# Kernel optimization log

Measured on AMD Instinct MI355X. Metric: run time of the kernel, lower is better.

Reference implementation:

```python
import jax, jax.numpy as jnp
import numpy as np

N_MEMBERS = 2      # ensemble_length=3, loop runs i=1..2
N_NODES = 65536    # batch_size * total_length = 32 * 2048
N_EDGES = 1_048_576
N_LAYERS = 12      # num_conv_layers
D = 64             # constant feature width (linspace 64->64)


def setup_inputs() -> dict:
    key = jax.random.key(0)
    k0, k1, k2, k3 = jax.random.split(key, 4)
    x = jax.random.normal(k0, (N_MEMBERS, N_NODES, D), dtype=jnp.float32)
    edge_index = jax.random.randint(k1, (N_MEMBERS, 2, N_EDGES), 0, N_NODES, dtype=jnp.int64)
    # GCNConv weights per member/layer; scale ~ 1/sqrt(D) for stability across 12 layers
    W = jax.random.normal(k2, (N_MEMBERS, N_LAYERS, D, D), dtype=jnp.float32) / jnp.sqrt(jnp.float32(D))
    b = jax.random.normal(k3, (N_MEMBERS, N_LAYERS, D), dtype=jnp.float32) * 0.01
    return {"x": x, "edge_index": edge_index, "W": W, "b": b}


def gcn_conv(h, src, dst, W, b):
    """PyG GCNConv: add self-loops, symmetric D^-1/2 (A+I) D^-1/2 normalization,
    linear transform, bias."""
    hw = h @ W                                                # [N, D_out]
    # degree includes the self-loop (+1)
    deg = jax.ops.segment_sum(jnp.ones((src.shape[0],), h.dtype), dst,
                              num_segments=N_NODES) + jnp.asarray(1.0, h.dtype)
    dinv = jax.lax.rsqrt(deg)                                 # [N]
    norm = dinv[src] * dinv[dst]                              # [E]
    agg = jax.ops.segment_sum(norm[:, None] * hw[src], dst, num_segments=N_NODES)
    agg = agg + (dinv * dinv)[:, None] * hw                   # self-loop term
    return agg + b


def reference(x, edge_index, W, b):
    # eval mode: F.dropout(training=False) is identity
    outs = []
    for i in range(N_MEMBERS):
        src, dst = edge_index[i, 0], edge_index[i, 1]
        h = x[i]
        for j in range(N_LAYERS - 1):
            h = jax.nn.relu(gcn_conv(h, src, dst, W[i, j], b[i, j]))
        outs.append(gcn_conv(h, src, dst, W[i, N_LAYERS - 1], b[i, N_LAYERS - 1]))
    return jnp.stack(outs)  # [N_MEMBERS, N_NODES, D]
```

## Files before the change

kernel.cpp:

```cpp
#include <hip/hip_runtime.h>
#include <hip/hip_fp16.h>
#include <math.h>

#define N_MEMBERS 2
#define N_NODES   65536
#define N_EDGES   1048576
#define N_LAYERS  12
#define D         64
#define OFF_STRIDE (N_NODES + 1)
#define NODE_MASK (N_NODES - 1)

#define NBINS       256
#define BIN_CAP     5120
#define EDGES_PER_WG 4096

typedef _Float16 f16;
typedef f16   f16x8 __attribute__((ext_vector_type(8)));
typedef float f32x4 __attribute__((ext_vector_type(4)));


__global__ __launch_bounds__(256) void bin_scatter_k(const int* __restrict__ ei,
                                                     int* __restrict__ binCursor,
                                                     unsigned int* __restrict__ binned) {
    int m = blockIdx.y;
    int t = threadIdx.x;
    int eBase = blockIdx.x * EDGES_PER_WG;
    __shared__ int hist[NBINS];
    __shared__ int base[NBINS];
    hist[t] = 0;
    __syncthreads();
    const int* srcp = ei + (size_t)(m * 2 + 0) * N_EDGES;
    const int* dstp = ei + (size_t)(m * 2 + 1) * N_EDGES;
    unsigned int pk[16];
    int bn[16], rk[16];
    #pragma unroll
    for (int i = 0; i < 16; i++) {
        int e = eBase + i * 256 + t;
        int src = srcp[e] & NODE_MASK;
        int dst = dstp[e] & NODE_MASK;
        int b = dst >> 8;
        bn[i] = b;
        pk[i] = ((unsigned)src << 8) | (unsigned)(dst & 255);
        rk[i] = atomicAdd(&hist[b], 1);
    }
    __syncthreads();
    base[t] = atomicAdd(&binCursor[m * NBINS + t], hist[t]);
    __syncthreads();
    unsigned int* bb = binned + (size_t)m * NBINS * BIN_CAP;
    #pragma unroll
    for (int i = 0; i < 16; i++) {
        int pos = base[bn[i]] + rk[i];
        if (pos < BIN_CAP)
            bb[(size_t)bn[i] * BIN_CAP + pos] = pk[i];
    }
}

__global__ __launch_bounds__(256) void scan_bins_k(const int* __restrict__ cur,
                                                   int* __restrict__ bbase) {
    int m = blockIdx.x, t = threadIdx.x;
    __shared__ int sh[256];
    int v0 = cur[m * NBINS + t];
    sh[t] = v0;
    __syncthreads();
    for (int ofs = 1; ofs < 256; ofs <<= 1) {
        int v = sh[t];
        int a = (t >= ofs) ? sh[t - ofs] : 0;
        __syncthreads();
        sh[t] = v + a;
        __syncthreads();
    }
    bbase[m * NBINS + t] = sh[t] - v0;
}

__global__ __launch_bounds__(256) void bin_build_k(const unsigned int* __restrict__ binned,
                                                   const int* __restrict__ binCursor,
                                                   const int* __restrict__ bbase,
                                                   int* __restrict__ off,
                                                   float* __restrict__ dinv,
                                                   unsigned short* __restrict__ csr_src) {
    int m = blockIdx.y, b = blockIdx.x, t = threadIdx.x;
    int cnt   = binCursor[m * NBINS + b];
    int gbase = bbase[m * NBINS + b];
    const unsigned int* bb = binned + ((size_t)m * NBINS + b) * BIN_CAP;
    __shared__ int degl[256];
    __shared__ int offl[256];
    degl[t] = 0;
    __syncthreads();
    unsigned int ed[20];
    #pragma unroll
    for (int j = 0; j < 20; j++) {
        int i = t + j * 256;
        ed[j] = 0;
        if (i < cnt) {
            unsigned int w = bb[i];
            int r = atomicAdd(&degl[w & 255], 1);
            ed[j] = w | ((unsigned)r << 24);
        }
    }
    __syncthreads();
    int myDeg = degl[t];
    offl[t] = myDeg;
    __syncthreads();
    for (int ofs = 1; ofs < 256; ofs <<= 1) {
        int v = offl[t];
        int a = (t >= ofs) ? offl[t - ofs] : 0;
        __syncthreads();
        offl[t] = v + a;
        __syncthreads();
    }
    int myOff = gbase + offl[t] - myDeg;
    int node = b * 256 + t;
    off[m * OFF_STRIDE + node] = myOff;
    if (b == NBINS - 1 && t == 255) off[m * OFF_STRIDE + N_NODES] = N_EDGES;
    dinv[m * N_NODES + node] = 1.0f / sqrtf((float)myDeg + 1.0f);
    offl[t] = myOff;
    __syncthreads();
    unsigned short* cs = csr_src + (size_t)m * N_EDGES;
    #pragma unroll
    for (int j = 0; j < 20; j++) {
        int i = t + j * 256;
        if (i < cnt) {
            int dl  = ed[j] & 255;
            int src = (ed[j] >> 8) & 0xFFFF;
            int r   = ed[j] >> 24;
            cs[offl[dl] + r] = (unsigned short)src;
        }
    }
}

__global__ __launch_bounds__(256) void prescale_k(const float* __restrict__ x,
                                                  const float* __restrict__ dinv,
                                                  __half* __restrict__ g) {
    int i = blockIdx.x * 256 + threadIdx.x;
    float dv = dinv[i >> 3];
    float4 a = ((const float4*)x)[i * 2];
    float4 b = ((const float4*)x)[i * 2 + 1];
    union { __half2 h2[4]; uint4 u; } p;
    p.h2[0] = __floats2half2_rn(dv * a.x, dv * a.y);
    p.h2[1] = __floats2half2_rn(dv * a.z, dv * a.w);
    p.h2[2] = __floats2half2_rn(dv * b.x, dv * b.y);
    p.h2[3] = __floats2half2_rn(dv * b.z, dv * b.w);
    ((uint4*)g)[i] = p.u;
}

__device__ __forceinline__ void cvt8(uint4 u, float* f) {
    const __half2* h2 = (const __half2*)&u;
    #pragma unroll
    for (int i = 0; i < 4; i++) {
        float2 t = __half22float2(h2[i]);
        f[2 * i]     = t.x;
        f[2 * i + 1] = t.y;
    }
}

__global__ __launch_bounds__(256) void aggregate_k(const __half* __restrict__ g,
                                                   __half* __restrict__ S,
                                                   const int* __restrict__ off,
                                                   const unsigned short* __restrict__ csr_src,
                                                   const float* __restrict__ dinv) {
    int m = blockIdx.y;
    int n = blockIdx.x * 4 + (threadIdx.x >> 6);
    int lane = threadIdx.x & 63;
    int fg   = lane & 7;
    int sub  = lane >> 3;
    const __half*         gm = g + (size_t)m * N_NODES * D;
    const int*            ob = off + m * OFF_STRIDE;
    const unsigned short* sb = csr_src + (size_t)m * N_EDGES;

    float acc[8];
    #pragma unroll
    for (int i = 0; i < 8; i++) acc[i] = 0.f;

    int e0 = ob[n], e1 = ob[n + 1];
    #pragma unroll 2
    for (int e = e0; e < e1; e += 8) {
        int ee  = e + sub;
        int idx = (ee < e1) ? ee : (e1 - 1);
        int s   = sb[idx];
        float w = (ee < e1) ? 1.0f : 0.0f;
        uint4 gv = *(const uint4*)(gm + (size_t)s * D + fg * 8);
        float f[8];
        cvt8(gv, f);
        #pragma unroll
        for (int i = 0; i < 8; i++) acc[i] = fmaf(w, f[i], acc[i]);
    }
    #pragma unroll
    for (int msk = 8; msk < 64; msk <<= 1)
        #pragma unroll
        for (int i = 0; i < 8; i++) acc[i] += __shfl_xor(acc[i], msk);

    float dv = dinv[m * N_NODES + n];
    uint4 sg = *(const uint4*)(gm + (size_t)n * D + fg * 8);
    float sf[8];
    cvt8(sg, sf);
    if (sub == 0) {
        union { __half2 h2[4]; uint4 u; } p;
        #pragma unroll
        for (int i = 0; i < 4; i++)
            p.h2[i] = __floats2half2_rn(dv * (acc[2 * i]     + sf[2 * i]),
                                        dv * (acc[2 * i + 1] + sf[2 * i + 1]));
        *(uint4*)(S + (size_t)m * N_NODES * D + (size_t)n * D + fg * 8) = p.u;
    }
}

__global__ __launch_bounds__(256) void gemm_f16_k(const __half* __restrict__ S,
                                                  const float* __restrict__ Wall,
                                                  const float* __restrict__ dinv,
                                                  const float* __restrict__ ball,
                                                  __half* __restrict__ gout,
                                                  float* __restrict__ fout,
                                                  int layer, int last) {
    int m = blockIdx.y;
    const float* Wg = Wall + (size_t)(m * N_LAYERS + layer) * D * D;
    __shared__ __align__(16) _Float16 Whi[D][72];
    __shared__ __align__(16) _Float16 Wlo[D][72];
    for (int idx = threadIdx.x; idx < D * D / 4; idx += 256) {
        float4 v = ((const float4*)Wg)[idx];
        int k  = idx >> 4;
        int c0 = (idx & 15) << 2;
        float vv[4] = {v.x, v.y, v.z, v.w};
        #pragma unroll
        for (int i = 0; i < 4; i++) {
            f16 hi = (f16)vv[i];
            Whi[c0 + i][k] = hi;
            Wlo[c0 + i][k] = (f16)(vv[i] - (float)hi);
        }
    }
    __syncthreads();

    int lane = threadIdx.x & 63;
    int wav  = threadIdx.x >> 6;
    int nn   = lane & 15;
    int quad = lane >> 4;

    f16x8 Bh[8], Bl[8];
    #pragma unroll
    for (int t = 0; t < 4; t++)
        #pragma unroll
        for (int s = 0; s < 2; s++) {
            Bh[t * 2 + s] = *(const f16x8*)&Whi[t * 16 + nn][s * 32 + quad * 8];
            Bl[t * 2 + s] = *(const f16x8*)&Wlo[t * 16 + nn][s * 32 + quad * 8];
        }

    const __half* Sm = S + (size_t)m * N_NODES * D;
    const float*  dm = dinv + m * N_NODES;
    const float*  bp = ball + (size_t)(m * N_LAYERS + layer) * D;
    __half*       gm = gout + (size_t)m * N_NODES * D;
    float*        fm = fout + (size_t)m * N_NODES * D;

    float bcol[4];
    #pragma unroll
    for (int t = 0; t < 4; t++) bcol[t] = bp[t * 16 + nn];

    int base = blockIdx.x * 256 + wav * 64;
    for (int g = 0; g < 4; g++) {
        int n0 = base + g * 16;
        const __half* srow = Sm + (size_t)(n0 + nn) * D;
        f16x8 a0 = *(const f16x8*)(srow + quad * 8);
        f16x8 a1 = *(const f16x8*)(srow + 32 + quad * 8);
        float dvr[4];
        #pragma unroll
        for (int r = 0; r < 4; r++) dvr[r] = dm[n0 + quad * 4 + r];
        #pragma unroll
        for (int t = 0; t < 4; t++) {
            f32x4 c = {0.f, 0.f, 0.f, 0.f};
            c = __builtin_amdgcn_mfma_f32_16x16x32_f16(a0, Bh[t * 2 + 0], c, 0, 0, 0);
            c = __builtin_amdgcn_mfma_f32_16x16x32_f16(a1, Bh[t * 2 + 1], c, 0, 0, 0);
            c = __builtin_amdgcn_mfma_f32_16x16x32_f16(a0, Bl[t * 2 + 0], c, 0, 0, 0);
            c = __builtin_amdgcn_mfma_f32_16x16x32_f16(a1, Bl[t * 2 + 1], c, 0, 0, 0);
            #pragma unroll
            for (int r = 0; r < 4; r++) {
                int row = n0 + quad * 4 + r;
                float v = (float)c[r] + bcol[t];
                if (last) {
                    fm[(size_t)row * D + t * 16 + nn] = v;
                } else {
                    gm[(size_t)row * D + t * 16 + nn] =
                        __float2half(fmaxf(v, 0.f) * dvr[r]);
                }
            }
        }
    }
}


extern "C" void kernel_launch(void* const* d_in, const int* in_sizes, int n_in,
                              void* d_out, int out_size, void* d_ws, size_t ws_size,
                              hipStream_t stream) {
    (void)in_sizes; (void)n_in; (void)out_size; (void)ws_size;
    const float* x  = (const float*)d_in[0];
    const int*   ei = (const int*)d_in[1];
    const float* W  = (const float*)d_in[2];
    const float* b  = (const float*)d_in[3];
    float* out = (float*)d_out;

    char* ws = (char*)d_ws;
    size_t o = 0;
    auto take = [&](size_t bytes) -> void* {
        void* p = ws + o;
        o = (o + bytes + 255) & ~(size_t)255;
        return p;
    };
    float*          dinv      = (float*) take((size_t)N_MEMBERS * N_NODES * 4);
    int*            off       = (int*)   take((size_t)N_MEMBERS * OFF_STRIDE * 4);
    int*            binCursor = (int*)   take((size_t)N_MEMBERS * NBINS * 4);
    int*            bbase     = (int*)   take((size_t)N_MEMBERS * NBINS * 4);
    unsigned short* csr_src   = (unsigned short*)take((size_t)N_MEMBERS * N_EDGES * 2);
    __half*         gbuf      = (__half*)take((size_t)N_MEMBERS * N_NODES * D * 2);
    __half*         Sbuf      = (__half*)take((size_t)N_MEMBERS * N_NODES * D * 2);
    unsigned int*   binned    = (unsigned int*)Sbuf;

    hipMemsetAsync(binCursor, 0, (size_t)N_MEMBERS * NBINS * 4, stream);

    bin_scatter_k<<<dim3(N_EDGES / EDGES_PER_WG, N_MEMBERS), 256, 0, stream>>>(
        ei, binCursor, binned);
    scan_bins_k<<<dim3(N_MEMBERS), 256, 0, stream>>>(binCursor, bbase);
    bin_build_k<<<dim3(NBINS, N_MEMBERS), 256, 0, stream>>>(
        binned, binCursor, bbase, off, dinv, csr_src);
    prescale_k<<<dim3((N_MEMBERS * N_NODES * D / 8) / 256), 256, 0, stream>>>(
        x, dinv, gbuf);

    for (int j = 0; j < N_LAYERS; j++) {
        aggregate_k<<<dim3(N_NODES / 4, N_MEMBERS), 256, 0, stream>>>(
            gbuf, Sbuf, off, csr_src, dinv);
        gemm_f16_k<<<dim3(N_NODES / 256, N_MEMBERS), 256, 0, stream>>>(
            Sbuf, W, dinv, b, gbuf, out, j, (j == N_LAYERS - 1) ? 1 : 0);
    }
}
```

Measured before the change: 915.1 us.

## Pin each member to an XCD group in aggregate and vectorize GEMM epilogue stores

The aggregate kernel now runs on a flat 1D grid whose block index is remapped so that each ensemble member lands on a fixed half of the eight XCDs (block index mod 8). The aim is to keep each member's gather working set in that half's L2 caches. The GEMM swaps the MFMA operand order so each lane owns four consecutive output columns of a single row. This allows float4 bias loads and 64/128-bit vector stores in place of scattered scalar stores. The XCD mapping relies on round-robin dispatch of blocks to XCDs.

After: 874.8 us. 4.4% less time.

```diff
diff --git a/kernel.cpp b/kernel.cpp
--- a/kernel.cpp
+++ b/kernel.cpp
@@ -158,8 +158,11 @@
                                                    const int* __restrict__ off,
                                                    const unsigned short* __restrict__ csr_src,
                                                    const float* __restrict__ dinv) {
-    int m = blockIdx.y;
-    int n = blockIdx.x * 4 + (threadIdx.x >> 6);
+    int bflat = blockIdx.x;
+    int xcd   = bflat & 7;
+    int m     = xcd >> 2;
+    int slot  = ((bflat >> 3) << 2) | (xcd & 3);
+    int n = slot * 4 + (threadIdx.x >> 6);
     int lane = threadIdx.x & 63;
     int fg   = lane & 7;
     int sub  = lane >> 3;
@@ -248,36 +251,37 @@
     __half*       gm = gout + (size_t)m * N_NODES * D;
     float*        fm = fout + (size_t)m * N_NODES * D;
 
-    float bcol[4];
-    #pragma unroll
-    for (int t = 0; t < 4; t++) bcol[t] = bp[t * 16 + nn];
+    float4 b4[4];
+    #pragma unroll
+    for (int t = 0; t < 4; t++)
+        b4[t] = *(const float4*)(bp + t * 16 + quad * 4);
 
     int base = blockIdx.x * 256 + wav * 64;
     for (int g = 0; g < 4; g++) {
-        int n0 = base + g * 16;
-        const __half* srow = Sm + (size_t)(n0 + nn) * D;
+        int node = base + g * 16 + nn;
+        const __half* srow = Sm + (size_t)node * D;
         f16x8 a0 = *(const f16x8*)(srow + quad * 8);
         f16x8 a1 = *(const f16x8*)(srow + 32 + quad * 8);
-        float dvr[4];
-        #pragma unroll
-        for (int r = 0; r < 4; r++) dvr[r] = dm[n0 + quad * 4 + r];
+        float dv = dm[node];
         #pragma unroll
         for (int t = 0; t < 4; t++) {
             f32x4 c = {0.f, 0.f, 0.f, 0.f};
-            c = __builtin_amdgcn_mfma_f32_16x16x32_f16(a0, Bh[t * 2 + 0], c, 0, 0, 0);
-            c = __builtin_amdgcn_mfma_f32_16x16x32_f16(a1, Bh[t * 2 + 1], c, 0, 0, 0);
-            c = __builtin_amdgcn_mfma_f32_16x16x32_f16(a0, Bl[t * 2 + 0], c, 0, 0, 0);
-            c = __builtin_amdgcn_mfma_f32_16x16x32_f16(a1, Bl[t * 2 + 1], c, 0, 0, 0);
-            #pragma unroll
-            for (int r = 0; r < 4; r++) {
-                int row = n0 + quad * 4 + r;
-                float v = (float)c[r] + bcol[t];
-                if (last) {
-                    fm[(size_t)row * D + t * 16 + nn] = v;
-                } else {
-                    gm[(size_t)row * D + t * 16 + nn] =
-                        __float2half(fmaxf(v, 0.f) * dvr[r]);
-                }
+            c = __builtin_amdgcn_mfma_f32_16x16x32_f16(Bh[t * 2 + 0], a0, c, 0, 0, 0);
+            c = __builtin_amdgcn_mfma_f32_16x16x32_f16(Bh[t * 2 + 1], a1, c, 0, 0, 0);
+            c = __builtin_amdgcn_mfma_f32_16x16x32_f16(Bl[t * 2 + 0], a0, c, 0, 0, 0);
+            c = __builtin_amdgcn_mfma_f32_16x16x32_f16(Bl[t * 2 + 1], a1, c, 0, 0, 0);
+            float v0 = (float)c[0] + b4[t].x;
+            float v1 = (float)c[1] + b4[t].y;
+            float v2 = (float)c[2] + b4[t].z;
+            float v3 = (float)c[3] + b4[t].w;
+            int col = t * 16 + quad * 4;
+            if (last) {
+                *(float4*)(fm + (size_t)node * D + col) = make_float4(v0, v1, v2, v3);
+            } else {
+                union { __half2 h2[2]; uint2 u; } p;
+                p.h2[0] = __floats2half2_rn(fmaxf(v0, 0.f) * dv, fmaxf(v1, 0.f) * dv);
+                p.h2[1] = __floats2half2_rn(fmaxf(v2, 0.f) * dv, fmaxf(v3, 0.f) * dv);
+                *(uint2*)(gm + (size_t)node * D + col) = p.u;
             }
         }
     }
@@ -321,7 +325,7 @@
         x, dinv, gbuf);
 
     for (int j = 0; j < N_LAYERS; j++) {
-        aggregate_k<<<dim3(N_NODES / 4, N_MEMBERS), 256, 0, stream>>>(
+        aggregate_k<<<dim3(N_MEMBERS * (N_NODES / 4)), 256, 0, stream>>>(
             gbuf, Sbuf, off, csr_src, dinv);
         gemm_f16_k<<<dim3(N_NODES / 256, N_MEMBERS), 256, 0, stream>>>(
             Sbuf, W, dinv, b, gbuf, out, j, (j == N_LAYERS - 1) ? 1 : 0);
```
